# Performance work log

Hardware: AMD Instinct MI355X
Metric: run time of the kernel (lower is better)

## Reference

```python
import jax, jax.numpy as jnp
import numpy as np

N, D, H, E, TOP_K = 4096, 1024, 2048, 8, 2


def setup_inputs() -> dict:
    key = jax.random.key(0)
    ks = jax.random.split(key, 8)
    s = 0.02
    return {
        "x": jax.random.normal(ks[0], (N, D), dtype=jnp.float32),
        "gate_W": jax.random.normal(ks[1], (D, E), dtype=jnp.float32) * s,
        "gate_b": jnp.zeros((E,), dtype=jnp.float32),
        "W1": jax.random.normal(ks[2], (E, D, H), dtype=jnp.float32) * s,
        "b1": jnp.zeros((E, H), dtype=jnp.float32),
        "W2": jax.random.normal(ks[3], (E, H, D), dtype=jnp.float32) * s,
        "b2": jnp.zeros((E, D), dtype=jnp.float32),
    }


def reference(x, gate_W, gate_b, W1, b1, W2, b2):
    # TopKGate: softmax over expert logits, pick top-k probs + indices.
    logits = x @ gate_W + gate_b                    # [N, E]
    probs = jax.nn.softmax(logits, axis=-1)
    gates, idxs = jax.lax.top_k(probs, TOP_K)        # [N, K] each

    # Combine weights w[n, e] = sum_k gates[n,k] * (idxs[n,k] == e).
    onehot = jax.nn.one_hot(idxs, E, dtype=x.dtype)  # [N, K, E]
    w = jnp.einsum("nke,nk->ne", onehot, gates)      # [N, E]

    # Dense per-expert MLP on all tokens; unrouted tokens get weight 0,
    # so the math matches the masked gather/scatter original exactly.
    h = jax.nn.relu(jnp.einsum("nd,edh->enh", x, W1) + b1[:, None, :])  # [E,N,H]
    y = jnp.einsum("enh,ehd->end", h, W2) + b2[:, None, :]               # [E,N,D]
    out = jnp.einsum("end,ne->nd", y, w)                                 # [N,D]
    return out
```

## Files before the change

### kernel.cpp

```cpp
#include <hip/hip_runtime.h>
#include <hip/hip_bf16.h>
#include <cstdint>

#define N_TOK 4096
#define DIM   1024
#define HID   2048
#define NE    8

typedef __bf16 bf16x8 __attribute__((ext_vector_type(8)));
typedef __bf16 bf16x4 __attribute__((ext_vector_type(4)));
typedef float  f32x4  __attribute__((ext_vector_type(4)));

__device__ __forceinline__ void gload16(const void* g, void* l) {
    __builtin_amdgcn_global_load_lds(
        (const __attribute__((address_space(1))) void*)g,
        (__attribute__((address_space(3))) void*)l, 16, 0, 0);
}

__global__ void cvt_x_kernel(const float* __restrict__ x, __bf16* __restrict__ xb) {
    const int i = (blockIdx.x * 256 + threadIdx.x) * 4;
    float4 v = *(const float4*)&x[i];
    bf16x4 o = { (__bf16)v.x, (__bf16)v.y, (__bf16)v.z, (__bf16)v.w };
    *(bf16x4*)&xb[i] = o;
}

__global__ void transpose_cvt_kernel(const float* __restrict__ src, __bf16* __restrict__ dst,
                                     int R, int C) {
    const size_t eoff = (size_t)blockIdx.z * R * C;
    src += eoff; dst += eoff;
    __shared__ float t[32][33];
    const int r0 = blockIdx.x * 32, c0 = blockIdx.y * 32;
    const int tr = threadIdx.x >> 3;
    const int tc = (threadIdx.x & 7) * 4;
    float4 v = *(const float4*)&src[(size_t)(r0 + tr) * C + c0 + tc];
    t[tr][tc + 0] = v.x; t[tr][tc + 1] = v.y; t[tr][tc + 2] = v.z; t[tr][tc + 3] = v.w;
    __syncthreads();
    bf16x4 o;
    o[0] = (__bf16)t[tc + 0][tr];
    o[1] = (__bf16)t[tc + 1][tr];
    o[2] = (__bf16)t[tc + 2][tr];
    o[3] = (__bf16)t[tc + 3][tr];
    *(bf16x4*)&dst[(size_t)(c0 + tr) * R + r0 + tc] = o;
}

__global__ void gate_kernel(const float* __restrict__ x, const float* __restrict__ gW,
                            const float* __restrict__ gb, int* __restrict__ top_idx,
                            float* __restrict__ top_gate) {
    const int tokn = blockIdx.x * 4 + (threadIdx.x >> 6);
    const int lane = threadIdx.x & 63;
    const float4* xr = (const float4*)(x + (size_t)tokn * DIM);
    float acc[NE] = {};
#pragma unroll
    for (int i = 0; i < 4; i++) {
        const int v4 = i * 64 + lane;
        const float4 xv = xr[v4];
        const float* wb = &gW[v4 * 4 * NE];
        const float xs[4] = { xv.x, xv.y, xv.z, xv.w };
#pragma unroll
        for (int j = 0; j < 4; j++) {
            const float4 wa = *(const float4*)&wb[j * NE];
            const float4 wc = *(const float4*)&wb[j * NE + 4];
            acc[0] += xs[j] * wa.x; acc[1] += xs[j] * wa.y;
            acc[2] += xs[j] * wa.z; acc[3] += xs[j] * wa.w;
            acc[4] += xs[j] * wc.x; acc[5] += xs[j] * wc.y;
            acc[6] += xs[j] * wc.z; acc[7] += xs[j] * wc.w;
        }
    }
#pragma unroll
    for (int e = 0; e < NE; e++)
#pragma unroll
        for (int s = 32; s > 0; s >>= 1)
            acc[e] += __shfl_down(acc[e], s, 64);
    if (lane == 0) {
        float lg[NE], p[NE];
        float mx = -1e30f;
#pragma unroll
        for (int e = 0; e < NE; e++) { lg[e] = acc[e] + gb[e]; mx = fmaxf(mx, lg[e]); }
        float s = 0.f;
#pragma unroll
        for (int e = 0; e < NE; e++) { p[e] = __expf(lg[e] - mx); s += p[e]; }
        const float inv = 1.f / s;
#pragma unroll
        for (int e = 0; e < NE; e++) p[e] *= inv;
        int i0 = 0; float p0 = p[0];
#pragma unroll
        for (int e = 1; e < NE; e++) if (p[e] > p0) { p0 = p[e]; i0 = e; }
        int i1 = -1; float p1 = -1.f;
#pragma unroll
        for (int e = 0; e < NE; e++) if (e != i0 && p[e] > p1) { p1 = p[e]; i1 = e; }
        top_idx[tokn * 2] = i0;  top_idx[tokn * 2 + 1] = i1;
        top_gate[tokn * 2] = p0; top_gate[tokn * 2 + 1] = p1;
    }
}

__global__ void count_kernel(const int* __restrict__ top_idx, int* __restrict__ cnt) {
    __shared__ int hist[NE];
    if (threadIdx.x < NE) hist[threadIdx.x] = 0;
    __syncthreads();
    const int n = blockIdx.x * 256 + threadIdx.x;
    atomicAdd(&hist[top_idx[n * 2]], 1);
    atomicAdd(&hist[top_idx[n * 2 + 1]], 1);
    __syncthreads();
    if (threadIdx.x < NE) atomicAdd(&cnt[threadIdx.x], hist[threadIdx.x]);
}

__global__ void scan_kernel(const int* __restrict__ cnt, int* __restrict__ offs) {
    if (threadIdx.x == 0) {
        int s = 0;
        for (int e = 0; e < NE; e++) { offs[e] = s; s += cnt[e]; }
        offs[NE] = s;
    }
}

__global__ void build_kernel(const int* __restrict__ top_idx, const int* __restrict__ offs,
                             int* __restrict__ run, int* __restrict__ row_token,
                             int* __restrict__ tok_row) {
    __shared__ int lrun[NE];
    __shared__ int base[NE];
    if (threadIdx.x < NE) lrun[threadIdx.x] = 0;
    __syncthreads();
    const int n = blockIdx.x * 256 + threadIdx.x;
    const int e0 = top_idx[n * 2], e1 = top_idx[n * 2 + 1];
    const int p0 = atomicAdd(&lrun[e0], 1);
    const int p1 = atomicAdd(&lrun[e1], 1);
    __syncthreads();
    if (threadIdx.x < NE) base[threadIdx.x] = atomicAdd(&run[threadIdx.x], lrun[threadIdx.x]);
    __syncthreads();
    const int r0 = offs[e0] + base[e0] + p0;
    const int r1 = offs[e1] + base[e1] + p1;
    row_token[r0] = n; tok_row[n * 2] = r0;
    row_token[r1] = n; tok_row[n * 2 + 1] = r1;
}

__global__ __launch_bounds__(256, 2) void gemm1_kernel(
    const __bf16* __restrict__ xb, const __bf16* __restrict__ w1t,
    const float* __restrict__ b1, const int* __restrict__ cnt,
    const int* __restrict__ offs, const int* __restrict__ row_token,
    __bf16* __restrict__ h) {
    const int lin = blockIdx.x;
    const int e   = lin & 7;
    const int t   = lin >> 3;
    const int mt  = t & 31;
    const int n0  = (t >> 5) * 128;
    const int ce  = cnt[e];
    if (mt * 128 >= ce) return;
    const int off_e = offs[e];

    __shared__ __bf16 lA[8192];
    __shared__ __bf16 lB[8192];

    const int tid  = threadIdx.x;
    const int lane = tid & 63;
    const int wid  = tid >> 6;
    const int quad = lane >> 4;
    const int l16  = lane & 15;
    const int wm   = wid & 1;
    const int wn   = wid >> 1;

    const int lrow = lane >> 3;
    const int cch  = (lane & 7) ^ lrow;
    const __bf16* aros[4]; const __bf16* bros[4];
    char* ldsA[4]; char* ldsB[4];
#pragma unroll
    for (int j = 0; j < 4; j++) {
        const int row = (wid * 4 + j) * 8 + lrow;
        int gr = off_e + mt * 128 + row;
        gr = gr < 2 * N_TOK - 1 ? gr : 2 * N_TOK - 1;
        const int tok = row_token[gr] & (N_TOK - 1);
        aros[j] = xb  + (size_t)tok * DIM + cch * 8;
        bros[j] = w1t + ((size_t)e * HID + n0 + row) * DIM + cch * 8;
        ldsA[j] = (char*)lA + (wid * 4 + j) * 1024;
        ldsB[j] = (char*)lB + (wid * 4 + j) * 1024;
    }

    f32x4 acc[4][4] = {};

    for (int kk = 0; kk < DIM; kk += 64) {
#pragma unroll
        for (int j = 0; j < 4; j++) gload16(aros[j] + kk, ldsA[j]);
#pragma unroll
        for (int j = 0; j < 4; j++) gload16(bros[j] + kk, ldsB[j]);
        __syncthreads();
#pragma unroll
        for (int hh = 0; hh < 2; hh++) {
            const int q4 = quad + hh * 4;
            const int sw = (q4 ^ (l16 & 7)) << 4;
            bf16x8 af[4], bfr[4];
#pragma unroll
            for (int mi = 0; mi < 4; mi++) {
                const int ar = wm * 64 + mi * 16 + l16;
                af[mi] = *(const bf16x8*)((const char*)lA + ar * 128 + sw);
            }
#pragma unroll
            for (int ni = 0; ni < 4; ni++) {
                const int br = wn * 64 + ni * 16 + l16;
                bfr[ni] = *(const bf16x8*)((const char*)lB + br * 128 + sw);
            }
#pragma unroll
            for (int mi = 0; mi < 4; mi++)
#pragma unroll
                for (int ni = 0; ni < 4; ni++)
                    acc[mi][ni] = __builtin_amdgcn_mfma_f32_16x16x32_bf16(af[mi], bfr[ni], acc[mi][ni], 0, 0, 0);
        }
        __syncthreads();
    }

#pragma unroll
    for (int ni = 0; ni < 4; ni++) {
        const int col = n0 + wn * 64 + ni * 16 + l16;
        const float bias = b1[e * HID + col];
#pragma unroll
        for (int mi = 0; mi < 4; mi++) {
#pragma unroll
            for (int r = 0; r < 4; r++) {
                const int lr = wm * 64 + mi * 16 + quad * 4 + r;
                const int gm = mt * 128 + lr;
                if (gm < ce) {
                    float v = acc[mi][ni][r] + bias;
                    v = v > 0.f ? v : 0.f;
                    h[(size_t)(off_e + gm) * HID + col] = (__bf16)v;
                }
            }
        }
    }
}

__global__ __launch_bounds__(256, 2) void gemm2_kernel(
    const __bf16* __restrict__ h, const __bf16* __restrict__ w2t,
    const float* __restrict__ b2, const int* __restrict__ cnt,
    const int* __restrict__ offs, float* __restrict__ y) {
    const int lin = blockIdx.x;
    const int e   = lin & 7;
    const int t   = lin >> 3;
    const int mt  = t & 31;
    const int n0  = (t >> 5) * 128;
    const int ce  = cnt[e];
    if (mt * 128 >= ce) return;
    const int off_e = offs[e];

    __shared__ __bf16 lA[8192];
    __shared__ __bf16 lB[8192];

    const int tid  = threadIdx.x;
    const int lane = tid & 63;
    const int wid  = tid >> 6;
    const int quad = lane >> 4;
    const int l16  = lane & 15;
    const int wm   = wid & 1;
    const int wn   = wid >> 1;

    const int lrow = lane >> 3;
    const int cch  = (lane & 7) ^ lrow;
    const __bf16* aros[4]; const __bf16* bros[4];
    char* ldsA[4]; char* ldsB[4];
#pragma unroll
    for (int j = 0; j < 4; j++) {
        const int row = (wid * 4 + j) * 8 + lrow;
        int gr = off_e + mt * 128 + row;
        gr = gr < 2 * N_TOK - 1 ? gr : 2 * N_TOK - 1;
        aros[j] = h   + (size_t)gr * HID + cch * 8;
        bros[j] = w2t + ((size_t)e * DIM + n0 + row) * HID + cch * 8;
        ldsA[j] = (char*)lA + (wid * 4 + j) * 1024;
        ldsB[j] = (char*)lB + (wid * 4 + j) * 1024;
    }

    f32x4 acc[4][4] = {};

    for (int kk = 0; kk < HID; kk += 64) {
#pragma unroll
        for (int j = 0; j < 4; j++) gload16(aros[j] + kk, ldsA[j]);
#pragma unroll
        for (int j = 0; j < 4; j++) gload16(bros[j] + kk, ldsB[j]);
        __syncthreads();
#pragma unroll
        for (int hh = 0; hh < 2; hh++) {
            const int q4 = quad + hh * 4;
            const int sw = (q4 ^ (l16 & 7)) << 4;
            bf16x8 af[4], bfr[4];
#pragma unroll
            for (int mi = 0; mi < 4; mi++) {
                const int ar = wm * 64 + mi * 16 + l16;
                af[mi] = *(const bf16x8*)((const char*)lA + ar * 128 + sw);
            }
#pragma unroll
            for (int ni = 0; ni < 4; ni++) {
                const int br = wn * 64 + ni * 16 + l16;
                bfr[ni] = *(const bf16x8*)((const char*)lB + br * 128 + sw);
            }
#pragma unroll
            for (int mi = 0; mi < 4; mi++)
#pragma unroll
                for (int ni = 0; ni < 4; ni++)
                    acc[mi][ni] = __builtin_amdgcn_mfma_f32_16x16x32_bf16(af[mi], bfr[ni], acc[mi][ni], 0, 0, 0);
        }
        __syncthreads();
    }

#pragma unroll
    for (int mi = 0; mi < 4; mi++) {
#pragma unroll
        for (int r = 0; r < 4; r++) {
            const int lr = wm * 64 + mi * 16 + quad * 4 + r;
            const int gm = mt * 128 + lr;
            if (gm < ce) {
#pragma unroll
                for (int ni = 0; ni < 4; ni++) {
                    const int col = n0 + wn * 64 + ni * 16 + l16;
                    y[(size_t)(off_e + gm) * DIM + col] = acc[mi][ni][r] + b2[e * DIM + col];
                }
            }
        }
    }
}

__global__ void combine_kernel(const float* __restrict__ y, const int* __restrict__ tok_row,
                               const float* __restrict__ top_gate, float* __restrict__ out) {
    const int n = blockIdx.x;
    const int d = threadIdx.x * 4;
    const int r0 = tok_row[n * 2], r1 = tok_row[n * 2 + 1];
    const float g0 = top_gate[n * 2], g1 = top_gate[n * 2 + 1];
    float4 a = *(const float4*)&y[(size_t)r0 * DIM + d];
    float4 b = *(const float4*)&y[(size_t)r1 * DIM + d];
    float4 o = { g0 * a.x + g1 * b.x, g0 * a.y + g1 * b.y,
                 g0 * a.z + g1 * b.z, g0 * a.w + g1 * b.w };
    *(float4*)&out[(size_t)n * DIM + d] = o;
}

extern "C" void kernel_launch(void* const* d_in, const int* in_sizes, int n_in,
                              void* d_out, int out_size, void* d_ws, size_t ws_size,
                              hipStream_t stream) {
    const float* x  = (const float*)d_in[0];
    const float* gW = (const float*)d_in[1];
    const float* gb = (const float*)d_in[2];
    const float* W1 = (const float*)d_in[3];
    const float* b1 = (const float*)d_in[4];
    const float* W2 = (const float*)d_in[5];
    const float* b2 = (const float*)d_in[6];
    float* out = (float*)d_out;

    char* ws = (char*)d_ws;
    __bf16* xb   = (__bf16*)(ws);
    __bf16* w1t  = (__bf16*)(ws + ((size_t)8  << 20));
    float*  ybuf = (float*) (ws + ((size_t)8  << 20));
    __bf16* w2t  = (__bf16*)(ws + ((size_t)40 << 20));
    __bf16* hbuf = (__bf16*)(ws + ((size_t)72 << 20));
    char* tail   = ws + ((size_t)104 << 20);
    int*   row_token = (int*)(tail);
    int*   tok_row   = (int*)(tail + 32768);
    int*   top_idx   = (int*)(tail + 65536);
    float* top_gate  = (float*)(tail + 98304);
    int*   cnt       = (int*)(tail + 131072);
    int*   offs      = cnt + 16;
    int*   run       = cnt + 32;

    hipMemsetAsync(cnt, 0, 256, stream);

    cvt_x_kernel<<<N_TOK * DIM / 4 / 256, 256, 0, stream>>>(x, xb);
    transpose_cvt_kernel<<<dim3(DIM / 32, HID / 32, NE), 256, 0, stream>>>(W1, w1t, DIM, HID);
    transpose_cvt_kernel<<<dim3(HID / 32, DIM / 32, NE), 256, 0, stream>>>(W2, w2t, HID, DIM);
    gate_kernel<<<N_TOK / 4, 256, 0, stream>>>(x, gW, gb, top_idx, top_gate);
    count_kernel<<<N_TOK / 256, 256, 0, stream>>>(top_idx, cnt);
    scan_kernel<<<1, 64, 0, stream>>>(cnt, offs);
    build_kernel<<<N_TOK / 256, 256, 0, stream>>>(top_idx, offs, run, row_token, tok_row);
    gemm1_kernel<<<NE * 32 * (HID / 128), 256, 0, stream>>>(xb, w1t, b1, cnt, offs, row_token, hbuf);
    gemm2_kernel<<<NE * 32 * (DIM / 128), 256, 0, stream>>>(hbuf, w2t, b2, cnt, offs, ybuf);
    combine_kernel<<<N_TOK, 256, 0, stream>>>(ybuf, tok_row, top_gate, out);
}
```

Measured before the change: 327.4 us.

## Fuse prep kernels and load GEMM weight fragments directly from global memory

The x-to-bf16 conversion is folded into the gate kernel, the scan kernel is merged into the build kernel, and the two weight-transpose launches become one. Both grouped GEMMs stop staging the weight tile in LDS. Each lane now reads its B fragments straight from global memory, while the A tile is staged with a deeper K step of 128 and a new swizzle. This removes several launches and halves LDS traffic and barriers per K, at the risk of uncoalesced or latency-exposed global reads for B that are repeated across M tiles.

```diff
diff --git a/kernel.cpp b/kernel.cpp
--- a/kernel.cpp
+++ b/kernel.cpp
@@ -17,19 +17,24 @@
         (__attribute__((address_space(3))) void*)l, 16, 0, 0);
 }
 
-__global__ void cvt_x_kernel(const float* __restrict__ x, __bf16* __restrict__ xb) {
-    const int i = (blockIdx.x * 256 + threadIdx.x) * 4;
-    float4 v = *(const float4*)&x[i];
-    bf16x4 o = { (__bf16)v.x, (__bf16)v.y, (__bf16)v.z, (__bf16)v.w };
-    *(bf16x4*)&xb[i] = o;
-}
-
-__global__ void transpose_cvt_kernel(const float* __restrict__ src, __bf16* __restrict__ dst,
-                                     int R, int C) {
-    const size_t eoff = (size_t)blockIdx.z * R * C;
-    src += eoff; dst += eoff;
+__global__ void transpose_cvt_all(const float* __restrict__ W1, const float* __restrict__ W2,
+                                  __bf16* __restrict__ w1t, __bf16* __restrict__ w2t) {
+    int lin = blockIdx.x;
+    const float* src; __bf16* dst; int R, C, rx, cy;
+    if (lin < 16384) {
+        const int e = lin >> 11, rem = lin & 2047;
+        rx = rem >> 6; cy = rem & 63;
+        R = DIM; C = HID;
+        src = W1 + (size_t)e * DIM * HID; dst = w1t + (size_t)e * DIM * HID;
+    } else {
+        lin -= 16384;
+        const int e = lin >> 11, rem = lin & 2047;
+        rx = rem >> 5; cy = rem & 31;
+        R = HID; C = DIM;
+        src = W2 + (size_t)e * DIM * HID; dst = w2t + (size_t)e * DIM * HID;
+    }
     __shared__ float t[32][33];
-    const int r0 = blockIdx.x * 32, c0 = blockIdx.y * 32;
+    const int r0 = rx * 32, c0 = cy * 32;
     const int tr = threadIdx.x >> 3;
     const int tc = (threadIdx.x & 7) * 4;
     float4 v = *(const float4*)&src[(size_t)(r0 + tr) * C + c0 + tc];
@@ -45,15 +50,18 @@
 
 __global__ void gate_kernel(const float* __restrict__ x, const float* __restrict__ gW,
                             const float* __restrict__ gb, int* __restrict__ top_idx,
-                            float* __restrict__ top_gate) {
+                            float* __restrict__ top_gate, __bf16* __restrict__ xb) {
     const int tokn = blockIdx.x * 4 + (threadIdx.x >> 6);
     const int lane = threadIdx.x & 63;
     const float4* xr = (const float4*)(x + (size_t)tokn * DIM);
+    __bf16* xbr = xb + (size_t)tokn * DIM;
     float acc[NE] = {};
 #pragma unroll
     for (int i = 0; i < 4; i++) {
         const int v4 = i * 64 + lane;
         const float4 xv = xr[v4];
+        bf16x4 xc = { (__bf16)xv.x, (__bf16)xv.y, (__bf16)xv.z, (__bf16)xv.w };
+        *(bf16x4*)&xbr[v4 * 4] = xc;
         const float* wb = &gW[v4 * 4 * NE];
         const float xs[4] = { xv.x, xv.y, xv.z, xv.w };
 #pragma unroll
@@ -104,19 +112,16 @@
     if (threadIdx.x < NE) atomicAdd(&cnt[threadIdx.x], hist[threadIdx.x]);
 }
 
-__global__ void scan_kernel(const int* __restrict__ cnt, int* __restrict__ offs) {
+__global__ void build_kernel(const int* __restrict__ top_idx, const int* __restrict__ cnt,
+                             int* __restrict__ run, int* __restrict__ row_token,
+                             int* __restrict__ tok_row) {
+    __shared__ int soffs[NE];
+    __shared__ int lrun[NE];
+    __shared__ int base[NE];
     if (threadIdx.x == 0) {
         int s = 0;
-        for (int e = 0; e < NE; e++) { offs[e] = s; s += cnt[e]; }
-        offs[NE] = s;
-    }
-}
-
-__global__ void build_kernel(const int* __restrict__ top_idx, const int* __restrict__ offs,
-                             int* __restrict__ run, int* __restrict__ row_token,
-                             int* __restrict__ tok_row) {
-    __shared__ int lrun[NE];
-    __shared__ int base[NE];
+        for (int e = 0; e < NE; e++) { soffs[e] = s; s += cnt[e]; }
+    }
     if (threadIdx.x < NE) lrun[threadIdx.x] = 0;
     __syncthreads();
     const int n = blockIdx.x * 256 + threadIdx.x;
@@ -126,8 +131,8 @@
     __syncthreads();
     if (threadIdx.x < NE) base[threadIdx.x] = atomicAdd(&run[threadIdx.x], lrun[threadIdx.x]);
     __syncthreads();
-    const int r0 = offs[e0] + base[e0] + p0;
-    const int r1 = offs[e1] + base[e1] + p1;
+    const int r0 = soffs[e0] + base[e0] + p0;
+    const int r1 = soffs[e1] + base[e1] + p1;
     row_token[r0] = n; tok_row[n * 2] = r0;
     row_token[r1] = n; tok_row[n * 2 + 1] = r1;
 }
@@ -135,19 +140,18 @@
 __global__ __launch_bounds__(256, 2) void gemm1_kernel(
     const __bf16* __restrict__ xb, const __bf16* __restrict__ w1t,
     const float* __restrict__ b1, const int* __restrict__ cnt,
-    const int* __restrict__ offs, const int* __restrict__ row_token,
-    __bf16* __restrict__ h) {
+    const int* __restrict__ row_token, __bf16* __restrict__ h) {
     const int lin = blockIdx.x;
     const int e   = lin & 7;
     const int t   = lin >> 3;
     const int mt  = t & 31;
     const int n0  = (t >> 5) * 128;
-    const int ce  = cnt[e];
+    int off_e = 0;
+    for (int i = 0; i < e; i++) off_e += cnt[i];
+    const int ce = cnt[e];
     if (mt * 128 >= ce) return;
-    const int off_e = offs[e];
-
-    __shared__ __bf16 lA[8192];
-    __shared__ __bf16 lB[8192];
+
+    __shared__ __bf16 lA[16384];
 
     const int tid  = threadIdx.x;
     const int lane = tid & 63;
@@ -157,45 +161,44 @@
     const int wm   = wid & 1;
     const int wn   = wid >> 1;
 
-    const int lrow = lane >> 3;
-    const int cch  = (lane & 7) ^ lrow;
-    const __bf16* aros[4]; const __bf16* bros[4];
-    char* ldsA[4]; char* ldsB[4];
-#pragma unroll
-    for (int j = 0; j < 4; j++) {
-        const int row = (wid * 4 + j) * 8 + lrow;
+    const int lrow = lane >> 4;
+    const int cc   = lane & 15;
+    const __bf16* aros[8];
+    char* ldsA[8];
+#pragma unroll
+    for (int j = 0; j < 8; j++) {
+        const int g   = wid * 8 + j;
+        const int row = g * 4 + lrow;
+        const int q   = cc ^ (((j & 1) << 2) | lrow);
         int gr = off_e + mt * 128 + row;
         gr = gr < 2 * N_TOK - 1 ? gr : 2 * N_TOK - 1;
         const int tok = row_token[gr] & (N_TOK - 1);
-        aros[j] = xb  + (size_t)tok * DIM + cch * 8;
-        bros[j] = w1t + ((size_t)e * HID + n0 + row) * DIM + cch * 8;
-        ldsA[j] = (char*)lA + (wid * 4 + j) * 1024;
-        ldsB[j] = (char*)lB + (wid * 4 + j) * 1024;
-    }
+        aros[j] = xb + (size_t)tok * DIM + q * 8;
+        ldsA[j] = (char*)lA + g * 1024;
+    }
+
+    const __bf16* bp[4];
+#pragma unroll
+    for (int ni = 0; ni < 4; ni++)
+        bp[ni] = w1t + ((size_t)e * HID + n0 + wn * 64 + ni * 16 + l16) * DIM + quad * 8;
 
     f32x4 acc[4][4] = {};
 
-    for (int kk = 0; kk < DIM; kk += 64) {
-#pragma unroll
-        for (int j = 0; j < 4; j++) gload16(aros[j] + kk, ldsA[j]);
-#pragma unroll
-        for (int j = 0; j < 4; j++) gload16(bros[j] + kk, ldsB[j]);
+    for (int kk = 0; kk < DIM; kk += 128) {
+#pragma unroll
+        for (int j = 0; j < 8; j++) gload16(aros[j] + kk, ldsA[j]);
         __syncthreads();
 #pragma unroll
-        for (int hh = 0; hh < 2; hh++) {
-            const int q4 = quad + hh * 4;
-            const int sw = (q4 ^ (l16 & 7)) << 4;
-            bf16x8 af[4], bfr[4];
-#pragma unroll
-            for (int mi = 0; mi < 4; mi++) {
-                const int ar = wm * 64 + mi * 16 + l16;
-                af[mi] = *(const bf16x8*)((const char*)lA + ar * 128 + sw);
-            }
-#pragma unroll
-            for (int ni = 0; ni < 4; ni++) {
-                const int br = wn * 64 + ni * 16 + l16;
-                bfr[ni] = *(const bf16x8*)((const char*)lB + br * 128 + sw);
-            }
+        for (int hh = 0; hh < 4; hh++) {
+            bf16x8 bfr[4];
+#pragma unroll
+            for (int ni = 0; ni < 4; ni++)
+                bfr[ni] = *(const bf16x8*)(bp[ni] + kk + hh * 32);
+            const int sw = (((hh * 4 + quad) ^ (l16 & 7)) << 4);
+            bf16x8 af[4];
+#pragma unroll
+            for (int mi = 0; mi < 4; mi++)
+                af[mi] = *(const bf16x8*)((const char*)lA + (wm * 64 + mi * 16 + l16) * 256 + sw);
 #pragma unroll
             for (int mi = 0; mi < 4; mi++)
 #pragma unroll
@@ -228,18 +231,18 @@
 __global__ __launch_bounds__(256, 2) void gemm2_kernel(
     const __bf16* __restrict__ h, const __bf16* __restrict__ w2t,
     const float* __restrict__ b2, const int* __restrict__ cnt,
-    const int* __restrict__ offs, float* __restrict__ y) {
+    float* __restrict__ y) {
     const int lin = blockIdx.x;
     const int e   = lin & 7;
     const int t   = lin >> 3;
     const int mt  = t & 31;
     const int n0  = (t >> 5) * 128;
-    const int ce  = cnt[e];
+    int off_e = 0;
+    for (int i = 0; i < e; i++) off_e += cnt[i];
+    const int ce = cnt[e];
     if (mt * 128 >= ce) return;
-    const int off_e = offs[e];
-
-    __shared__ __bf16 lA[8192];
-    __shared__ __bf16 lB[8192];
+
+    __shared__ __bf16 lA[16384];
 
     const int tid  = threadIdx.x;
     const int lane = tid & 63;
@@ -249,44 +252,43 @@
     const int wm   = wid & 1;
     const int wn   = wid >> 1;
 
-    const int lrow = lane >> 3;
-    const int cch  = (lane & 7) ^ lrow;
-    const __bf16* aros[4]; const __bf16* bros[4];
-    char* ldsA[4]; char* ldsB[4];
-#pragma unroll
-    for (int j = 0; j < 4; j++) {
-        const int row = (wid * 4 + j) * 8 + lrow;
+    const int lrow = lane >> 4;
+    const int cc   = lane & 15;
+    const __bf16* aros[8];
+    char* ldsA[8];
+#pragma unroll
+    for (int j = 0; j < 8; j++) {
+        const int g   = wid * 8 + j;
+        const int row = g * 4 + lrow;
+        const int q   = cc ^ (((j & 1) << 2) | lrow);
         int gr = off_e + mt * 128 + row;
         gr = gr < 2 * N_TOK - 1 ? gr : 2 * N_TOK - 1;
-        aros[j] = h   + (size_t)gr * HID + cch * 8;
-        bros[j] = w2t + ((size_t)e * DIM + n0 + row) * HID + cch * 8;
-        ldsA[j] = (char*)lA + (wid * 4 + j) * 1024;
-        ldsB[j] = (char*)lB + (wid * 4 + j) * 1024;
-    }
+        aros[j] = h + (size_t)gr * HID + q * 8;
+        ldsA[j] = (char*)lA + g * 1024;
+    }
+
+    const __bf16* bp[4];
+#pragma unroll
+    for (int ni = 0; ni < 4; ni++)
+        bp[ni] = w2t + ((size_t)e * DIM + n0 + wn * 64 + ni * 16 + l16) * HID + quad * 8;
 
     f32x4 acc[4][4] = {};
 
-    for (int kk = 0; kk < HID; kk += 64) {
-#pragma unroll
-        for (int j = 0; j < 4; j++) gload16(aros[j] + kk, ldsA[j]);
-#pragma unroll
-        for (int j = 0; j < 4; j++) gload16(bros[j] + kk, ldsB[j]);
+    for (int kk = 0; kk < HID; kk += 128) {
+#pragma unroll
+        for (int j = 0; j < 8; j++) gload16(aros[j] + kk, ldsA[j]);
         __syncthreads();
 #pragma unroll
-        for (int hh = 0; hh < 2; hh++) {
-            const int q4 = quad + hh * 4;
-            const int sw = (q4 ^ (l16 & 7)) << 4;
-            bf16x8 af[4], bfr[4];
-#pragma unroll
-            for (int mi = 0; mi < 4; mi++) {
-                const int ar = wm * 64 + mi * 16 + l16;
-                af[mi] = *(const bf16x8*)((const char*)lA + ar * 128 + sw);
-            }
-#pragma unroll
-            for (int ni = 0; ni < 4; ni++) {
-                const int br = wn * 64 + ni * 16 + l16;
-                bfr[ni] = *(const bf16x8*)((const char*)lB + br * 128 + sw);
-            }
+        for (int hh = 0; hh < 4; hh++) {
+            bf16x8 bfr[4];
+#pragma unroll
+            for (int ni = 0; ni < 4; ni++)
+                bfr[ni] = *(const bf16x8*)(bp[ni] + kk + hh * 32);
+            const int sw = (((hh * 4 + quad) ^ (l16 & 7)) << 4);
+            bf16x8 af[4];
+#pragma unroll
+            for (int mi = 0; mi < 4; mi++)
+                af[mi] = *(const bf16x8*)((const char*)lA + (wm * 64 + mi * 16 + l16) * 256 + sw);
 #pragma unroll
             for (int mi = 0; mi < 4; mi++)
 #pragma unroll
@@ -350,19 +352,15 @@
     int*   top_idx   = (int*)(tail + 65536);
     float* top_gate  = (float*)(tail + 98304);
     int*   cnt       = (int*)(tail + 131072);
-    int*   offs      = cnt + 16;
     int*   run       = cnt + 32;
 
     hipMemsetAsync(cnt, 0, 256, stream);
 
-    cvt_x_kernel<<<N_TOK * DIM / 4 / 256, 256, 0, stream>>>(x, xb);
-    transpose_cvt_kernel<<<dim3(DIM / 32, HID / 32, NE), 256, 0, stream>>>(W1, w1t, DIM, HID);
-    transpose_cvt_kernel<<<dim3(HID / 32, DIM / 32, NE), 256, 0, stream>>>(W2, w2t, HID, DIM);
-    gate_kernel<<<N_TOK / 4, 256, 0, stream>>>(x, gW, gb, top_idx, top_gate);
+    gate_kernel<<<N_TOK / 4, 256, 0, stream>>>(x, gW, gb, top_idx, top_gate, xb);
     count_kernel<<<N_TOK / 256, 256, 0, stream>>>(top_idx, cnt);
-    scan_kernel<<<1, 64, 0, stream>>>(cnt, offs);
-    build_kernel<<<N_TOK / 256, 256, 0, stream>>>(top_idx, offs, run, row_token, tok_row);
-    gemm1_kernel<<<NE * 32 * (HID / 128), 256, 0, stream>>>(xb, w1t, b1, cnt, offs, row_token, hbuf);
-    gemm2_kernel<<<NE * 32 * (DIM / 128), 256, 0, stream>>>(hbuf, w2t, b2, cnt, offs, ybuf);
+    build_kernel<<<N_TOK / 256, 256, 0, stream>>>(top_idx, cnt, run, row_token, tok_row);
+    transpose_cvt_all<<<32768, 256, 0, stream>>>(W1, W2, w1t, w2t);
+    gemm1_kernel<<<NE * 32 * (HID / 128), 256, 0, stream>>>(xb, w1t, b1, cnt, row_token, hbuf);
+    gemm2_kernel<<<NE * 32 * (DIM / 128), 256, 0, stream>>>(hbuf, w2t, b2, cnt, ybuf);
     combine_kernel<<<N_TOK, 256, 0, stream>>>(ybuf, tok_row, top_gate, out);
 }
```

New measurement: 435.2 us. +32.9%, slower.
